# Optimization experiments

Hardware: AMD Instinct MI355X
Metric: run time of the kernel (lower is better)

Reference implementation:

```python
import jax, jax.numpy as jnp
import numpy as np

OUT_F = 8192
IN_F = 8192
RANK = 32
N_TOK = 128


def _pack_ternary(w_q):
    """Pack int8 ternary {-1,0,+1} [out,in] -> uint8 [out,in//4], LSB-first 2-bit codes."""
    enc = (w_q.astype(np.int32) + 1).astype(np.uint8).reshape(w_q.shape[0], -1, 4)
    packed = enc[:, :, 0] | (enc[:, :, 1] << 2) | (enc[:, :, 2] << 4) | (enc[:, :, 3] << 6)
    return packed


def setup_inputs() -> dict:
    key = jax.random.key(0)
    kx, kw, ks, ka, kb, kbias = jax.random.split(key, 6)
    x = jax.random.normal(kx, (N_TOK, IN_F), dtype=jnp.float32)
    # ternary weights in {-1,0,+1}
    w_q = np.asarray(jax.random.randint(kw, (OUT_F, IN_F), -1, 2, dtype=jnp.int32), dtype=np.int8)
    weight_packed = jnp.asarray(_pack_ternary(w_q), dtype=jnp.uint8)
    scale = jax.random.uniform(ks, (OUT_F,), dtype=jnp.float32, minval=0.01, maxval=0.05)
    lora_A = jax.random.normal(ka, (OUT_F, RANK), dtype=jnp.float32) * 0.02
    lora_B = jax.random.normal(kb, (RANK, IN_F), dtype=jnp.float32) * 0.02
    bias = jax.random.normal(kbias, (OUT_F,), dtype=jnp.float32) * 0.01
    return {"x": x, "weight_packed": weight_packed, "scale": scale,
            "lora_A": lora_A, "lora_B": lora_B, "bias": bias, "in_features": IN_F}


def _unpack_ternary(packed, in_features, dtype):
    # packed: uint8 [out, in//4]; LSB-first 2-bit codes, code-1 -> {-1,0,+1}
    p = packed.astype(jnp.int32)
    vals = jnp.stack([p & 3, (p >> 2) & 3, (p >> 4) & 3, (p >> 6) & 3], axis=-1)
    vals = vals.reshape(packed.shape[0], -1)[:, :in_features] - 1
    return vals.astype(dtype)


def reference(x, weight_packed, scale, lora_A, lora_B, bias, in_features):
    W = _unpack_ternary(weight_packed, in_features, x.dtype)  # [out, in]
    out = (x @ W.T) * scale[None, :]                          # [n, out]
    out = out + (x @ lora_B.T) @ lora_A.T                     # low-rank LoRA path
    out = out + bias
    return out
```

## Files before the change

kernel.cpp:

```cpp
#include <hip/hip_runtime.h>
#include <hip/hip_bf16.h>
#include <stdint.h>

typedef float f32x4 __attribute__((ext_vector_type(4)));
typedef __bf16 bf16x8 __attribute__((ext_vector_type(8)));
typedef unsigned short ushort8 __attribute__((ext_vector_type(8)));

typedef const __attribute__((address_space(1))) uint32_t gu32;
typedef __attribute__((address_space(3))) uint32_t lu32;

#define N_TOK 128
#define OUT_F 8192
#define IN_F  8192
#define RANK  32

#define KSPLIT 8
#define KB    (IN_F / KSPLIT)
#define BK    64
#define NSTEP (KB / BK)
#define WSTRIDE 16
#define LKC   4

#define XB_OFF 0
#define TB_OFF ((size_t)N_TOK * IN_F * 2)
#define PO_OFF (TB_OFF + (size_t)LKC * N_TOK * RANK * 4)

__device__ __forceinline__ unsigned short bf16r(float f) {
    uint32_t u = __float_as_uint(f);
    return (unsigned short)((u + 0x7FFFu + ((u >> 16) & 1u)) >> 16);
}

__device__ __forceinline__ int swz(int row, int col) { return col ^ ((row & 7) << 3); }

__global__ __launch_bounds__(256) void cvt_x(const float* __restrict__ x,
                                             unsigned short* __restrict__ xt) {
    size_t f = (size_t)blockIdx.x * 256 + threadIdx.x;
    int c8 = (int)(f & 7);
    int r = (int)((f >> 3) & 127);
    int sblk = (int)(f >> 10);
    int k = sblk * 64 + ((c8 ^ (r & 7)) << 3);
    const float4* sp = (const float4*)(x + (size_t)r * IN_F + k);
    float4 a = sp[0], b = sp[1];
    ushort8 o;
    o[0] = bf16r(a.x); o[1] = bf16r(a.y); o[2] = bf16r(a.z); o[3] = bf16r(a.w);
    o[4] = bf16r(b.x); o[5] = bf16r(b.y); o[6] = bf16r(b.z); o[7] = bf16r(b.w);
    *(ushort8*)(xt + f * 8) = o;
}

__global__ __launch_bounds__(256) void lora_t(const float* __restrict__ x,
                                              const float* __restrict__ lb,
                                              float* __restrict__ tB) {
    __shared__ float ts[256][33];
    __shared__ float ps[8][32];
    const int m = blockIdx.x >> 2, kc = blockIdx.x & 3;
    const int tid = threadIdx.x;
    const int c0 = kc * 2048 + tid * 8;
    float4 xv0 = *(const float4*)(x + (size_t)m * IN_F + c0);
    float4 xv1 = *(const float4*)(x + (size_t)m * IN_F + c0 + 4);
#pragma unroll
    for (int r = 0; r < RANK; ++r) {
        const float4* bp = (const float4*)(lb + (size_t)r * IN_F + c0);
        float4 b0 = bp[0], b1 = bp[1];
        float s = xv0.x * b0.x + xv0.y * b0.y + xv0.z * b0.z + xv0.w * b0.w +
                  xv1.x * b1.x + xv1.y * b1.y + xv1.z * b1.z + xv1.w * b1.w;
        ts[tid][r] = s;
    }
    __syncthreads();
    {
        int g = tid >> 5, r = tid & 31;
        float s = 0.f;
        for (int j = 0; j < 32; ++j) s += ts[g * 32 + j][r];
        ps[g][r] = s;
    }
    __syncthreads();
    if (tid < 32) {
        float s = 0.f;
#pragma unroll
        for (int g = 0; g < 8; ++g) s += ps[g][tid];
        tB[(kc * N_TOK + m) * RANK + tid] = s;
    }
}

__device__ __forceinline__ void decodeW(int4 v, uint32_t d[8]) {
    uint32_t p = (uint32_t)v.x | ((uint32_t)v.y << 8) |
                 ((uint32_t)v.z << 16) | ((uint32_t)v.w << 24);
    const uint32_t HI = 0x403F00BFu;
    const uint32_t LO = 0x00800080u;
#pragma unroll
    for (int j = 0; j < 8; ++j) {
        uint32_t c0 = (p >> (4 * j)) & 3u;
        uint32_t c1 = (p >> (4 * j + 2)) & 3u;
        uint32_t t = c0 | (c1 << 16);
        uint32_t sel = (t | (t << 8)) + 0x04000400u;
        d[j] = __builtin_amdgcn_perm(HI, LO, sel);
    }
}

__global__ __launch_bounds__(256) void ternary_gemm(const unsigned short* __restrict__ xt,
                                                    const int* __restrict__ wp,
                                                    unsigned short* __restrict__ pO) {
    __shared__ unsigned short xs[2][128][64];
    __shared__ unsigned short ww[2][128][64];
    const int tid = threadIdx.x;
    const int nb = blockIdx.x >> 3;
    const int ks = blockIdx.x & 7;
    const int n0 = nb * 128;
    const int lane = tid & 63;
    const int wid = tid >> 6;
    const int wr = wid >> 1, wc = wid & 1;

    const int srow = tid >> 2;
    const int xcol = (tid & 3) * 16;
    const int* pg0 = wp + (size_t)(n0 + srow) * (IN_F / 4) + ks * (KB / 4) + (tid & 3) * 4;
    const int* pg1 = pg0 + (size_t)64 * (IN_F / 4);

    const unsigned short* xsrc = xt + ((size_t)(ks * NSTEP) * 128 + wid * 8) * 64 + lane * 8;

    f32x4 acc[4][4];
#pragma unroll
    for (int i = 0; i < 4; ++i)
#pragma unroll
        for (int j = 0; j < 4; ++j) acc[i][j] = (f32x4){0.f, 0.f, 0.f, 0.f};

    const int arow = lane & 15;
    const int kgrp = (lane >> 4) * 8;
    const int wc0 = swz(srow, xcol), wc1 = swz(srow, xcol + 8);

#pragma unroll
    for (int j = 0; j < 4; ++j)
        __builtin_amdgcn_global_load_lds(
            (gu32*)(xsrc + j * 2048),
            (lu32*)((char*)(&xs[0][0][0]) + wid * 1024 + j * 4096), 16, 0, 0);
    __builtin_amdgcn_sched_barrier(0);
    int4 wA0 = *(const int4*)(pg0);
    int4 wA1 = *(const int4*)(pg1);
    __builtin_amdgcn_sched_barrier(0);
    int4 wB0 = *(const int4*)(pg0 + WSTRIDE);
    int4 wB1 = *(const int4*)(pg1 + WSTRIDE);
    __builtin_amdgcn_sched_barrier(0);
    {
        uint32_t d0[8], d1[8];
        decodeW(wA0, d0);
        decodeW(wA1, d1);
        *(uint4*)&ww[0][srow][wc0]      = make_uint4(d0[0], d0[1], d0[2], d0[3]);
        *(uint4*)&ww[0][srow][wc1]      = make_uint4(d0[4], d0[5], d0[6], d0[7]);
        *(uint4*)&ww[0][srow + 64][wc0] = make_uint4(d1[0], d1[1], d1[2], d1[3]);
        *(uint4*)&ww[0][srow + 64][wc1] = make_uint4(d1[4], d1[5], d1[6], d1[7]);
    }
    __builtin_amdgcn_sched_barrier(0);
    asm volatile("s_waitcnt lgkmcnt(0)" ::: "memory");
    __builtin_amdgcn_s_barrier();
    __builtin_amdgcn_sched_barrier(0);

#pragma unroll
    for (int s = 0; s < NSTEP; ++s) {
        const int cur = s & 1, nxt = cur ^ 1;
        if (s + 1 < NSTEP) {
#pragma unroll
            for (int j = 0; j < 4; ++j)
                __builtin_amdgcn_global_load_lds(
                    (gu32*)(xsrc + (size_t)(s + 1) * 8192 + j * 2048),
                    (lu32*)((char*)(&xs[nxt][0][0]) + wid * 1024 + j * 4096), 16, 0, 0);
        }
        __builtin_amdgcn_sched_barrier(0);
        if (s + 2 < NSTEP) {
            if ((s & 1) == 0) {
                wA0 = *(const int4*)(pg0 + (s + 2) * WSTRIDE);
                wA1 = *(const int4*)(pg1 + (s + 2) * WSTRIDE);
            } else {
                wB0 = *(const int4*)(pg0 + (s + 2) * WSTRIDE);
                wB1 = *(const int4*)(pg1 + (s + 2) * WSTRIDE);
            }
        }
        __builtin_amdgcn_sched_barrier(0);
        if (s + 1 < NSTEP) {
            uint32_t d0[8], d1[8];
            if ((s & 1) == 0) { decodeW(wB0, d0); decodeW(wB1, d1); }
            else              { decodeW(wA0, d0); decodeW(wA1, d1); }
            *(uint4*)&ww[nxt][srow][wc0]      = make_uint4(d0[0], d0[1], d0[2], d0[3]);
            *(uint4*)&ww[nxt][srow][wc1]      = make_uint4(d0[4], d0[5], d0[6], d0[7]);
            *(uint4*)&ww[nxt][srow + 64][wc0] = make_uint4(d1[0], d1[1], d1[2], d1[3]);
            *(uint4*)&ww[nxt][srow + 64][wc1] = make_uint4(d1[4], d1[5], d1[6], d1[7]);
        }
#pragma unroll
        for (int kk = 0; kk < 2; ++kk) {
            const int kcol = kk * 32 + kgrp;
            bf16x8 af[4], bfr[4];
#pragma unroll
            for (int ar = 0; ar < 4; ++ar) {
                int row = wr * 64 + ar * 16 + arow;
                af[ar] = *(const bf16x8*)&xs[cur][row][swz(row, kcol)];
            }
#pragma unroll
            for (int br = 0; br < 4; ++br) {
                int row = wc * 64 + br * 16 + arow;
                bfr[br] = *(const bf16x8*)&ww[cur][row][swz(row, kcol)];
            }
#pragma unroll
            for (int ar = 0; ar < 4; ++ar)
#pragma unroll
                for (int br = 0; br < 4; ++br)
                    acc[ar][br] = __builtin_amdgcn_mfma_f32_16x16x32_bf16(
                        af[ar], bfr[br], acc[ar][br], 0, 0, 0);
        }
        if (s + 1 < NSTEP) {
            __builtin_amdgcn_sched_barrier(0);
            if (s + 2 < NSTEP) {
                asm volatile("s_waitcnt vmcnt(2) lgkmcnt(0)" ::: "memory");
            } else {
                asm volatile("s_waitcnt vmcnt(0) lgkmcnt(0)" ::: "memory");
            }
            __builtin_amdgcn_s_barrier();
            __builtin_amdgcn_sched_barrier(0);
        }
    }

    unsigned short* po = pO + ((size_t)ks << 20);
    const int mrow = (lane >> 4) * 4;
#pragma unroll
    for (int ar = 0; ar < 4; ++ar) {
#pragma unroll
        for (int br = 0; br < 4; ++br) {
            int m = wr * 64 + ar * 16 + mrow;
            int n = n0 + wc * 64 + br * 16 + arow;
            unsigned short* pp = po + (size_t)m * OUT_F + n;
#pragma unroll
            for (int j = 0; j < 4; ++j) pp[(size_t)j * OUT_F] = bf16r(acc[ar][br][j]);
        }
    }
}

__global__ __launch_bounds__(256) void reduce_out(const unsigned short* __restrict__ pO,
                                                  const float* __restrict__ tB,
                                                  const float* __restrict__ scale,
                                                  const float* __restrict__ lora_A,
                                                  const float* __restrict__ bias,
                                                  float* __restrict__ out) {
    __shared__ float ts[4][RANK];
    int nb = blockIdx.x & 15, mg = blockIdx.x >> 4;
    int tid = threadIdx.x;
    int m0 = mg * 4;
    if (tid < 128) {
        int i = tid >> 5, r = tid & 31;
        float s = 0.f;
#pragma unroll
        for (int c = 0; c < LKC; ++c) s += tB[(c * N_TOK + m0 + i) * RANK + r];
        ts[i][r] = s;
    }
    __syncthreads();
    int n = nb * 512 + tid * 2;
    float sc0 = scale[n], sc1 = scale[n + 1];
    float bs0 = bias[n], bs1 = bias[n + 1];
    float4 a0[8], a1[8];
    const float4* ap0 = (const float4*)(lora_A + (size_t)n * RANK);
    const float4* ap1 = (const float4*)(lora_A + (size_t)(n + 1) * RANK);
#pragma unroll
    for (int q = 0; q < 8; ++q) { a0[q] = ap0[q]; a1[q] = ap1[q]; }
#pragma unroll
    for (int i = 0; i < 4; ++i) {
        int m = m0 + i;
        const unsigned short* pp = pO + (size_t)m * OUT_F + n;
        float s0 = 0.f, s1 = 0.f;
#pragma unroll
        for (int c = 0; c < KSPLIT; ++c) {
            uint32_t u = *(const uint32_t*)(pp + ((size_t)c << 20));
            s0 += __uint_as_float(u << 16);
            s1 += __uint_as_float(u & 0xFFFF0000u);
        }
        float l0 = 0.f, l1 = 0.f;
#pragma unroll
        for (int q = 0; q < 8; ++q) {
            float4 tv = *(const float4*)&ts[i][q * 4];
            l0 = fmaf(tv.x, a0[q].x, l0); l0 = fmaf(tv.y, a0[q].y, l0);
            l0 = fmaf(tv.z, a0[q].z, l0); l0 = fmaf(tv.w, a0[q].w, l0);
            l1 = fmaf(tv.x, a1[q].x, l1); l1 = fmaf(tv.y, a1[q].y, l1);
            l1 = fmaf(tv.z, a1[q].z, l1); l1 = fmaf(tv.w, a1[q].w, l1);
        }
        out[(size_t)m * OUT_F + n]     = fmaf(s0, sc0, l0 + bs0);
        out[(size_t)m * OUT_F + n + 1] = fmaf(s1, sc1, l1 + bs1);
    }
}

extern "C" void kernel_launch(void* const* d_in, const int* in_sizes, int n_in,
                              void* d_out, int out_size, void* d_ws, size_t ws_size,
                              hipStream_t stream) {
    const float* x      = (const float*)d_in[0];
    const int*   wp     = (const int*)d_in[1];
    const float* scale  = (const float*)d_in[2];
    const float* lora_A = (const float*)d_in[3];
    const float* lora_B = (const float*)d_in[4];
    const float* bias   = (const float*)d_in[5];
    float* out = (float*)d_out;

    char* ws = (char*)d_ws;
    unsigned short* xt = (unsigned short*)(ws + XB_OFF);
    float* tB = (float*)(ws + TB_OFF);
    unsigned short* pO = (unsigned short*)(ws + PO_OFF);

    cvt_x<<<512, 256, 0, stream>>>(x, xt);
    lora_t<<<N_TOK * LKC, 256, 0, stream>>>(x, lora_B, tB);
    ternary_gemm<<<(OUT_F / 128) * KSPLIT, 256, 0, stream>>>(xt, wp, pO);
    reduce_out<<<16 * 32, 256, 0, stream>>>(pO, tB, scale, lora_A, bias, out);
}
```

Before: 52.78 us.

## Deepen prefetch pipeline: triple-buffer x tiles and four-deep weight register prefetch

Triple-buffers the activation tile in LDS, so the async global-to-LDS copies run two steps ahead instead of one, and keeps four sets of packed weight registers prefetched four steps ahead instead of two. The vmcnt waits are retuned per step to match the deeper queue of outstanding loads. The MFMA section is also wrapped in s_setprio raises. The aim is to hide more global memory latency, at the cost of more LDS, more VGPRs, and hand-counted waits that break silently if the load counts change.

```diff
diff --git a/kernel.cpp b/kernel.cpp
--- a/kernel.cpp
+++ b/kernel.cpp
@@ -99,7 +99,7 @@
 __global__ __launch_bounds__(256) void ternary_gemm(const unsigned short* __restrict__ xt,
                                                     const int* __restrict__ wp,
                                                     unsigned short* __restrict__ pO) {
-    __shared__ unsigned short xs[2][128][64];
+    __shared__ unsigned short xs[3][128][64];
     __shared__ unsigned short ww[2][128][64];
     const int tid = threadIdx.x;
     const int nb = blockIdx.x >> 3;
@@ -126,27 +126,39 @@
     const int kgrp = (lane >> 4) * 8;
     const int wc0 = swz(srow, xcol), wc1 = swz(srow, xcol + 8);
 
-#pragma unroll
-    for (int j = 0; j < 4; ++j)
-        __builtin_amdgcn_global_load_lds(
-            (gu32*)(xsrc + j * 2048),
-            (lu32*)((char*)(&xs[0][0][0]) + wid * 1024 + j * 4096), 16, 0, 0);
-    __builtin_amdgcn_sched_barrier(0);
-    int4 wA0 = *(const int4*)(pg0);
-    int4 wA1 = *(const int4*)(pg1);
-    __builtin_amdgcn_sched_barrier(0);
-    int4 wB0 = *(const int4*)(pg0 + WSTRIDE);
-    int4 wB1 = *(const int4*)(pg1 + WSTRIDE);
-    __builtin_amdgcn_sched_barrier(0);
-    {
-        uint32_t d0[8], d1[8];
-        decodeW(wA0, d0);
-        decodeW(wA1, d1);
-        *(uint4*)&ww[0][srow][wc0]      = make_uint4(d0[0], d0[1], d0[2], d0[3]);
-        *(uint4*)&ww[0][srow][wc1]      = make_uint4(d0[4], d0[5], d0[6], d0[7]);
-        *(uint4*)&ww[0][srow + 64][wc0] = make_uint4(d1[0], d1[1], d1[2], d1[3]);
-        *(uint4*)&ww[0][srow + 64][wc1] = make_uint4(d1[4], d1[5], d1[6], d1[7]);
-    }
+    int4 wreg[4][2];
+
+#define DMA_STEP(t, buf)                                                          \
+    {                                                                             \
+        _Pragma("unroll")                                                         \
+        for (int j = 0; j < 4; ++j)                                               \
+            __builtin_amdgcn_global_load_lds(                                     \
+                (gu32*)(xsrc + (size_t)(t) * 8192 + j * 2048),                    \
+                (lu32*)((char*)(&xs[(buf)][0][0]) + wid * 1024 + j * 4096), 16, 0, 0); \
+    }
+
+#define STAGE_WW(set, buf)                                                        \
+    {                                                                             \
+        uint32_t d0[8], d1[8];                                                    \
+        decodeW(wreg[(set)][0], d0);                                              \
+        decodeW(wreg[(set)][1], d1);                                              \
+        *(uint4*)&ww[(buf)][srow][wc0]      = make_uint4(d0[0], d0[1], d0[2], d0[3]); \
+        *(uint4*)&ww[(buf)][srow][wc1]      = make_uint4(d0[4], d0[5], d0[6], d0[7]); \
+        *(uint4*)&ww[(buf)][srow + 64][wc0] = make_uint4(d1[0], d1[1], d1[2], d1[3]); \
+        *(uint4*)&ww[(buf)][srow + 64][wc1] = make_uint4(d1[4], d1[5], d1[6], d1[7]); \
+    }
+
+    DMA_STEP(0, 0);
+    __builtin_amdgcn_sched_barrier(0);
+    DMA_STEP(1, 1);
+    __builtin_amdgcn_sched_barrier(0);
+#pragma unroll
+    for (int t = 0; t < 4; ++t) {
+        wreg[t][0] = *(const int4*)(pg0 + t * WSTRIDE);
+        wreg[t][1] = *(const int4*)(pg1 + t * WSTRIDE);
+    }
+    __builtin_amdgcn_sched_barrier(0);
+    STAGE_WW(0, 0);
     __builtin_amdgcn_sched_barrier(0);
     asm volatile("s_waitcnt lgkmcnt(0)" ::: "memory");
     __builtin_amdgcn_s_barrier();
@@ -154,34 +166,15 @@
 
 #pragma unroll
     for (int s = 0; s < NSTEP; ++s) {
-        const int cur = s & 1, nxt = cur ^ 1;
-        if (s + 1 < NSTEP) {
-#pragma unroll
-            for (int j = 0; j < 4; ++j)
-                __builtin_amdgcn_global_load_lds(
-                    (gu32*)(xsrc + (size_t)(s + 1) * 8192 + j * 2048),
-                    (lu32*)((char*)(&xs[nxt][0][0]) + wid * 1024 + j * 4096), 16, 0, 0);
-        }
+        if (s + 2 < NSTEP) DMA_STEP(s + 2, (s + 2) % 3);
         __builtin_amdgcn_sched_barrier(0);
-        if (s + 2 < NSTEP) {
-            if ((s & 1) == 0) {
-                wA0 = *(const int4*)(pg0 + (s + 2) * WSTRIDE);
-                wA1 = *(const int4*)(pg1 + (s + 2) * WSTRIDE);
-            } else {
-                wB0 = *(const int4*)(pg0 + (s + 2) * WSTRIDE);
-                wB1 = *(const int4*)(pg1 + (s + 2) * WSTRIDE);
-            }
+        if (s + 4 < NSTEP) {
+            wreg[s & 3][0] = *(const int4*)(pg0 + (s + 4) * WSTRIDE);
+            wreg[s & 3][1] = *(const int4*)(pg1 + (s + 4) * WSTRIDE);
         }
         __builtin_amdgcn_sched_barrier(0);
-        if (s + 1 < NSTEP) {
-            uint32_t d0[8], d1[8];
-            if ((s & 1) == 0) { decodeW(wB0, d0); decodeW(wB1, d1); }
-            else              { decodeW(wA0, d0); decodeW(wA1, d1); }
-            *(uint4*)&ww[nxt][srow][wc0]      = make_uint4(d0[0], d0[1], d0[2], d0[3]);
-            *(uint4*)&ww[nxt][srow][wc1]      = make_uint4(d0[4], d0[5], d0[6], d0[7]);
-            *(uint4*)&ww[nxt][srow + 64][wc0] = make_uint4(d1[0], d1[1], d1[2], d1[3]);
-            *(uint4*)&ww[nxt][srow + 64][wc1] = make_uint4(d1[4], d1[5], d1[6], d1[7]);
-        }
+        if (s + 1 < NSTEP) STAGE_WW((s + 1) & 3, (s + 1) & 1);
+        __builtin_amdgcn_s_setprio(1);
 #pragma unroll
         for (int kk = 0; kk < 2; ++kk) {
             const int kcol = kk * 32 + kgrp;
@@ -189,12 +182,12 @@
 #pragma unroll
             for (int ar = 0; ar < 4; ++ar) {
                 int row = wr * 64 + ar * 16 + arow;
-                af[ar] = *(const bf16x8*)&xs[cur][row][swz(row, kcol)];
+                af[ar] = *(const bf16x8*)&xs[s % 3][row][swz(row, kcol)];
             }
 #pragma unroll
             for (int br = 0; br < 4; ++br) {
                 int row = wc * 64 + br * 16 + arow;
-                bfr[br] = *(const bf16x8*)&ww[cur][row][swz(row, kcol)];
+                bfr[br] = *(const bf16x8*)&ww[s & 1][row][swz(row, kcol)];
             }
 #pragma unroll
             for (int ar = 0; ar < 4; ++ar)
@@ -203,17 +196,20 @@
                     acc[ar][br] = __builtin_amdgcn_mfma_f32_16x16x32_bf16(
                         af[ar], bfr[br], acc[ar][br], 0, 0, 0);
         }
+        __builtin_amdgcn_s_setprio(0);
         if (s + 1 < NSTEP) {
             __builtin_amdgcn_sched_barrier(0);
-            if (s + 2 < NSTEP) {
-                asm volatile("s_waitcnt vmcnt(2) lgkmcnt(0)" ::: "memory");
-            } else {
-                asm volatile("s_waitcnt vmcnt(0) lgkmcnt(0)" ::: "memory");
-            }
+            if (s == 0)       asm volatile("s_waitcnt vmcnt(10) lgkmcnt(0)" ::: "memory");
+            else if (s <= 11) asm volatile("s_waitcnt vmcnt(8) lgkmcnt(0)" ::: "memory");
+            else if (s == 12) asm volatile("s_waitcnt vmcnt(6) lgkmcnt(0)" ::: "memory");
+            else if (s == 13) asm volatile("s_waitcnt vmcnt(4) lgkmcnt(0)" ::: "memory");
+            else              asm volatile("s_waitcnt vmcnt(0) lgkmcnt(0)" ::: "memory");
             __builtin_amdgcn_s_barrier();
             __builtin_amdgcn_sched_barrier(0);
         }
     }
+#undef DMA_STEP
+#undef STAGE_WW
 
     unsigned short* po = pO + ((size_t)ks << 20);
     const int mrow = (lane >> 4) * 4;
```

New measurement: 51.56 us. 1.02x faster.

## Load activations directly into registers in MFMA fragment order, single-buffer weight LDS

Applied to the files above, without the earlier changes.

The activation conversion kernel now writes bf16 x in per-lane MFMA fragment order, so the GEMM loads A fragments straight from global memory into registers, double-buffered across steps, instead of staging them through LDS with global_load_lds. Weight tiles use a single LDS buffer guarded by an extra barrier before each overwrite. The aim is to halve LDS traffic and footprint and remove the LDS reads for A. In exchange it adds register pressure, a second barrier per step, and exposes global-load latency on the A operand.

```diff
diff --git a/kernel.cpp b/kernel.cpp
--- a/kernel.cpp
+++ b/kernel.cpp
@@ -5,9 +5,6 @@
 typedef float f32x4 __attribute__((ext_vector_type(4)));
 typedef __bf16 bf16x8 __attribute__((ext_vector_type(8)));
 typedef unsigned short ushort8 __attribute__((ext_vector_type(8)));
-
-typedef const __attribute__((address_space(1))) uint32_t gu32;
-typedef __attribute__((address_space(3))) uint32_t lu32;
 
 #define N_TOK 128
 #define OUT_F 8192
@@ -35,11 +32,14 @@
 __global__ __launch_bounds__(256) void cvt_x(const float* __restrict__ x,
                                              unsigned short* __restrict__ xt) {
     size_t f = (size_t)blockIdx.x * 256 + threadIdx.x;
-    int c8 = (int)(f & 7);
-    int r = (int)((f >> 3) & 127);
-    int sblk = (int)(f >> 10);
-    int k = sblk * 64 + ((c8 ^ (r & 7)) << 3);
-    const float4* sp = (const float4*)(x + (size_t)r * IN_F + k);
+    int lane = (int)(f & 63);
+    int rec  = (int)(f >> 6);
+    int ar16 = rec & 7;
+    int kk   = (rec >> 3) & 1;
+    int sblk = rec >> 4;
+    int row = ar16 * 16 + (lane & 15);
+    int k   = sblk * 64 + kk * 32 + (lane >> 4) * 8;
+    const float4* sp = (const float4*)(x + (size_t)row * IN_F + k);
     float4 a = sp[0], b = sp[1];
     ushort8 o;
     o[0] = bf16r(a.x); o[1] = bf16r(a.y); o[2] = bf16r(a.z); o[3] = bf16r(a.w);
@@ -99,8 +99,7 @@
 __global__ __launch_bounds__(256) void ternary_gemm(const unsigned short* __restrict__ xt,
                                                     const int* __restrict__ wp,
                                                     unsigned short* __restrict__ pO) {
-    __shared__ unsigned short xs[2][128][64];
-    __shared__ unsigned short ww[2][128][64];
+    __shared__ unsigned short ww[128][64];
     const int tid = threadIdx.x;
     const int nb = blockIdx.x >> 3;
     const int ks = blockIdx.x & 7;
@@ -114,39 +113,43 @@
     const int* pg0 = wp + (size_t)(n0 + srow) * (IN_F / 4) + ks * (KB / 4) + (tid & 3) * 4;
     const int* pg1 = pg0 + (size_t)64 * (IN_F / 4);
 
-    const unsigned short* xsrc = xt + ((size_t)(ks * NSTEP) * 128 + wid * 8) * 64 + lane * 8;
-
-    f32x4 acc[4][4];
-#pragma unroll
-    for (int i = 0; i < 4; ++i)
-#pragma unroll
-        for (int j = 0; j < 4; ++j) acc[i][j] = (f32x4){0.f, 0.f, 0.f, 0.f};
-
     const int arow = lane & 15;
     const int kgrp = (lane >> 4) * 8;
     const int wc0 = swz(srow, xcol), wc1 = swz(srow, xcol + 8);
 
-#pragma unroll
-    for (int j = 0; j < 4; ++j)
-        __builtin_amdgcn_global_load_lds(
-            (gu32*)(xsrc + j * 2048),
-            (lu32*)((char*)(&xs[0][0][0]) + wid * 1024 + j * 4096), 16, 0, 0);
-    __builtin_amdgcn_sched_barrier(0);
-    int4 wA0 = *(const int4*)(pg0);
-    int4 wA1 = *(const int4*)(pg1);
-    __builtin_amdgcn_sched_barrier(0);
-    int4 wB0 = *(const int4*)(pg0 + WSTRIDE);
-    int4 wB1 = *(const int4*)(pg1 + WSTRIDE);
-    __builtin_amdgcn_sched_barrier(0);
+    const unsigned short* abase = xt + ((size_t)(ks * NSTEP) * 16) * 512 + lane * 8;
+#define LDA(s_, kk_, ar_) \
+    (*(const bf16x8*)(abase + ((size_t)((s_)*16 + (kk_)*8 + (wr * 4 + (ar_)))) * 512))
+
+    f32x4 acc[4][4];
+#pragma unroll
+    for (int i = 0; i < 4; ++i)
+#pragma unroll
+        for (int j = 0; j < 4; ++j) acc[i][j] = (f32x4){0.f, 0.f, 0.f, 0.f};
+
+    bf16x8 aX[4][2], aY[4][2];
+    int4 wP[2][2];
+
+#pragma unroll
+    for (int ar = 0; ar < 4; ++ar) {
+        aX[ar][0] = LDA(0, 0, ar);
+        aX[ar][1] = LDA(0, 1, ar);
+    }
+    wP[0][0] = *(const int4*)(pg0);
+    wP[0][1] = *(const int4*)(pg1);
+    wP[1][0] = *(const int4*)(pg0 + WSTRIDE);
+    wP[1][1] = *(const int4*)(pg1 + WSTRIDE);
     {
         uint32_t d0[8], d1[8];
-        decodeW(wA0, d0);
-        decodeW(wA1, d1);
-        *(uint4*)&ww[0][srow][wc0]      = make_uint4(d0[0], d0[1], d0[2], d0[3]);
-        *(uint4*)&ww[0][srow][wc1]      = make_uint4(d0[4], d0[5], d0[6], d0[7]);
-        *(uint4*)&ww[0][srow + 64][wc0] = make_uint4(d1[0], d1[1], d1[2], d1[3]);
-        *(uint4*)&ww[0][srow + 64][wc1] = make_uint4(d1[4], d1[5], d1[6], d1[7]);
-    }
+        decodeW(wP[0][0], d0);
+        decodeW(wP[0][1], d1);
+        *(uint4*)&ww[srow][wc0]      = make_uint4(d0[0], d0[1], d0[2], d0[3]);
+        *(uint4*)&ww[srow][wc1]      = make_uint4(d0[4], d0[5], d0[6], d0[7]);
+        *(uint4*)&ww[srow + 64][wc0] = make_uint4(d1[0], d1[1], d1[2], d1[3]);
+        *(uint4*)&ww[srow + 64][wc1] = make_uint4(d1[4], d1[5], d1[6], d1[7]);
+    }
+    wP[0][0] = *(const int4*)(pg0 + 2 * WSTRIDE);
+    wP[0][1] = *(const int4*)(pg1 + 2 * WSTRIDE);
     __builtin_amdgcn_sched_barrier(0);
     asm volatile("s_waitcnt lgkmcnt(0)" ::: "memory");
     __builtin_amdgcn_s_barrier();
@@ -154,66 +157,51 @@
 
 #pragma unroll
     for (int s = 0; s < NSTEP; ++s) {
-        const int cur = s & 1, nxt = cur ^ 1;
-        if (s + 1 < NSTEP) {
-#pragma unroll
-            for (int j = 0; j < 4; ++j)
-                __builtin_amdgcn_global_load_lds(
-                    (gu32*)(xsrc + (size_t)(s + 1) * 8192 + j * 2048),
-                    (lu32*)((char*)(&xs[nxt][0][0]) + wid * 1024 + j * 4096), 16, 0, 0);
-        }
-        __builtin_amdgcn_sched_barrier(0);
-        if (s + 2 < NSTEP) {
-            if ((s & 1) == 0) {
-                wA0 = *(const int4*)(pg0 + (s + 2) * WSTRIDE);
-                wA1 = *(const int4*)(pg1 + (s + 2) * WSTRIDE);
-            } else {
-                wB0 = *(const int4*)(pg0 + (s + 2) * WSTRIDE);
-                wB1 = *(const int4*)(pg1 + (s + 2) * WSTRIDE);
+        bf16x8 (*aCur)[2] = (s & 1) ? aY : aX;
+        bf16x8 (*aNxt)[2] = (s & 1) ? aX : aY;
+        bf16x8 bfr[2][4];
+#pragma unroll
+        for (int kk = 0; kk < 2; ++kk)
+#pragma unroll
+            for (int br = 0; br < 4; ++br) {
+                int row = wc * 64 + br * 16 + arow;
+                bfr[kk][br] = *(const bf16x8*)&ww[row][swz(row, kk * 32 + kgrp)];
             }
-        }
-        __builtin_amdgcn_sched_barrier(0);
+#pragma unroll
+        for (int ar = 0; ar < 4; ++ar) {
+#pragma unroll
+            for (int kk = 0; kk < 2; ++kk)
+#pragma unroll
+                for (int br = 0; br < 4; ++br)
+                    acc[ar][br] = __builtin_amdgcn_mfma_f32_16x16x32_bf16(
+                        aCur[ar][kk], bfr[kk][br], acc[ar][br], 0, 0, 0);
+            if (s + 1 < NSTEP) {
+                aNxt[ar][0] = LDA(s + 1, 0, ar);
+                aNxt[ar][1] = LDA(s + 1, 1, ar);
+            }
+        }
         if (s + 1 < NSTEP) {
             uint32_t d0[8], d1[8];
-            if ((s & 1) == 0) { decodeW(wB0, d0); decodeW(wB1, d1); }
-            else              { decodeW(wA0, d0); decodeW(wA1, d1); }
-            *(uint4*)&ww[nxt][srow][wc0]      = make_uint4(d0[0], d0[1], d0[2], d0[3]);
-            *(uint4*)&ww[nxt][srow][wc1]      = make_uint4(d0[4], d0[5], d0[6], d0[7]);
-            *(uint4*)&ww[nxt][srow + 64][wc0] = make_uint4(d1[0], d1[1], d1[2], d1[3]);
-            *(uint4*)&ww[nxt][srow + 64][wc1] = make_uint4(d1[4], d1[5], d1[6], d1[7]);
-        }
-#pragma unroll
-        for (int kk = 0; kk < 2; ++kk) {
-            const int kcol = kk * 32 + kgrp;
-            bf16x8 af[4], bfr[4];
-#pragma unroll
-            for (int ar = 0; ar < 4; ++ar) {
-                int row = wr * 64 + ar * 16 + arow;
-                af[ar] = *(const bf16x8*)&xs[cur][row][swz(row, kcol)];
+            decodeW(wP[(s + 1) & 1][0], d0);
+            decodeW(wP[(s + 1) & 1][1], d1);
+            __builtin_amdgcn_sched_barrier(0);
+            __builtin_amdgcn_s_barrier();
+            __builtin_amdgcn_sched_barrier(0);
+            *(uint4*)&ww[srow][wc0]      = make_uint4(d0[0], d0[1], d0[2], d0[3]);
+            *(uint4*)&ww[srow][wc1]      = make_uint4(d0[4], d0[5], d0[6], d0[7]);
+            *(uint4*)&ww[srow + 64][wc0] = make_uint4(d1[0], d1[1], d1[2], d1[3]);
+            *(uint4*)&ww[srow + 64][wc1] = make_uint4(d1[4], d1[5], d1[6], d1[7]);
+            if (s + 2 < NSTEP) {
+                wP[s & 1][0] = *(const int4*)(pg0 + (s + 2) * WSTRIDE);
+                wP[s & 1][1] = *(const int4*)(pg1 + (s + 2) * WSTRIDE);
             }
-#pragma unroll
-            for (int br = 0; br < 4; ++br) {
-                int row = wc * 64 + br * 16 + arow;
-                bfr[br] = *(const bf16x8*)&ww[cur][row][swz(row, kcol)];
-            }
-#pragma unroll
-            for (int ar = 0; ar < 4; ++ar)
-#pragma unroll
-                for (int br = 0; br < 4; ++br)
-                    acc[ar][br] = __builtin_amdgcn_mfma_f32_16x16x32_bf16(
-                        af[ar], bfr[br], acc[ar][br], 0, 0, 0);
-        }
-        if (s + 1 < NSTEP) {
-            __builtin_amdgcn_sched_barrier(0);
-            if (s + 2 < NSTEP) {
-                asm volatile("s_waitcnt vmcnt(2) lgkmcnt(0)" ::: "memory");
-            } else {
-                asm volatile("s_waitcnt vmcnt(0) lgkmcnt(0)" ::: "memory");
-            }
+            __builtin_amdgcn_sched_barrier(0);
+            asm volatile("s_waitcnt lgkmcnt(0)" ::: "memory");
             __builtin_amdgcn_s_barrier();
             __builtin_amdgcn_sched_barrier(0);
         }
     }
+#undef LDA
 
     unsigned short* po = pO + ((size_t)ks << 20);
     const int mrow = (lane >> 4) * 4;
```

Measured after the change: 49.61 us (median of 4 runs). 1.06x faster.
